# Kernel tuning notes

Measured on AMD Instinct MI355X. Metric: run time of the kernel, lower is better.

The kernel has to match this reference:

```python
import jax, jax.numpy as jnp
import numpy as np

N_NODES = 20000
N_EDGES = 320000
IN_F = 256
HID = 64
OUT_F = 64
EDGE_F = 16
HEADS = 4
NUM_CLASSES = 10
NUM_GRAPHS = 40
ALPHA = 0.2  # LeakyReLU negative slope


def _xavier(key, shape):
    fan_in, fan_out = shape[0], shape[-1]
    std = 1.414 * np.sqrt(2.0 / (fan_in + fan_out))
    return jax.random.normal(key, shape, dtype=jnp.float32) * std


def setup_inputs() -> dict:
    key = jax.random.key(0)
    ks = jax.random.split(key, 12)
    x = jax.random.normal(ks[0], (N_NODES, IN_F), dtype=jnp.float32)
    edge_index = jax.random.randint(ks[1], (2, N_EDGES), 0, N_NODES, dtype=jnp.int32)
    edge_attr = jax.random.uniform(ks[2], (N_EDGES, EDGE_F), dtype=jnp.float32)
    batch = jnp.sort(jax.random.randint(ks[3], (N_NODES,), 0, NUM_GRAPHS, dtype=jnp.int32))
    # layer 0: in=IN_F, heads=HEADS, out=HID, concat
    W0 = _xavier(ks[4], (IN_F, HEADS * HID))
    a0 = _xavier(ks[5], (HEADS, 2 * HID + EDGE_F))
    # layer 1: in=HID*HEADS, heads=HEADS, out=HID, concat
    W1 = _xavier(ks[6], (HID * HEADS, HEADS * HID))
    a1 = _xavier(ks[7], (HEADS, 2 * HID + EDGE_F))
    # layer 2: in=HID*HEADS, heads=1, out=OUT_F, mean over heads
    W2 = _xavier(ks[8], (HID * HEADS, 1 * OUT_F))
    a2 = _xavier(ks[9], (1, 2 * OUT_F + EDGE_F))
    cls_w = _xavier(ks[10], (OUT_F, NUM_CLASSES))
    cls_b = jnp.zeros((NUM_CLASSES,), dtype=jnp.float32)
    return {"x": x, "edge_index": edge_index, "edge_attr": edge_attr, "batch": batch,
            "W0": W0, "a0": a0, "W1": W1, "a1": a1, "W2": W2, "a2": a2,
            "cls_w": cls_w, "cls_b": cls_b}


def gat_layer(h, W, a, edge_index, edge_attr, heads, out_f, concat):
    n = h.shape[0]
    Wh = (h @ W).reshape(n, heads, out_f)              # [N,H,D]
    src, dst = edge_index[0], edge_index[1]
    a_i, a_j, a_e = a[:, :out_f], a[:, out_f:2 * out_f], a[:, 2 * out_f:]
    # per-node head scores, gathered per edge (equivalent to concat + dot with a)
    s_i = jnp.einsum('nhd,hd->nh', Wh, a_i)            # [N,H]
    s_j = jnp.einsum('nhd,hd->nh', Wh, a_j)            # [N,H]
    s_e = edge_attr @ a_e.T                            # [E,H]
    e = s_i[src] + s_j[dst] + s_e                      # [E,H]
    e = jnp.where(e > 0, e, ALPHA * e)                 # LeakyReLU
    # NB: faithful to source — softmax over the HEADS dim (dim=1), not per-node
    att = jax.nn.softmax(e, axis=1)                    # [E,H]
    msg = att[:, :, None] * Wh[dst]                    # [E,H,D]
    h_prime = jax.ops.segment_sum(msg, src, num_segments=n)  # scatter-add to src
    if concat:
        return jax.nn.elu(h_prime.reshape(n, heads * out_f))
    return h_prime.mean(axis=1)


def reference(x, edge_index, edge_attr, batch, W0, a0, W1, a1, W2, a2, cls_w, cls_b):
    h = gat_layer(x, W0, a0, edge_index, edge_attr, HEADS, HID, True)
    h = gat_layer(h, W1, a1, edge_index, edge_attr, HEADS, HID, True)
    h = gat_layer(h, W2, a2, edge_index, edge_attr, 1, OUT_F, False)
    # global mean pool over graphs
    sums = jax.ops.segment_sum(h, batch, num_segments=NUM_GRAPHS)
    cnts = jax.ops.segment_sum(jnp.ones((h.shape[0],), h.dtype), batch, num_segments=NUM_GRAPHS)
    pooled = sums / jnp.maximum(cnts, 1.0)[:, None]
    logits = pooled @ cls_w + cls_b
    return jax.nn.log_softmax(logits, axis=1)
```

## Files before the change

### kernel.cpp

```cpp
#include <hip/hip_runtime.h>
#include <hip/hip_bf16.h>
#include <math.h>

#define N_NODES 20000
#define N_EDGES 320000
#define IN_F 256
#define HID 64
#define HEADS 4
#define OUT_F 64
#define EDGE_F 16
#define NUM_CLASSES 10
#define NUM_GRAPHS 40
#define LRELU_ALPHA 0.2f

typedef short bf16x8 __attribute__((ext_vector_type(8)));
typedef unsigned short u16x8 __attribute__((ext_vector_type(8)));
typedef float f32x4 __attribute__((ext_vector_type(4)));

static __device__ __forceinline__ float bf2f(unsigned short u) {
    union { unsigned int i; float f; } v; v.i = ((unsigned int)u) << 16; return v.f;
}
static __device__ __forceinline__ unsigned short f2bf(float f) {
    union { float f; unsigned int i; } v; v.f = f;
    unsigned int r = v.i + 0x7FFF + ((v.i >> 16) & 1);
    return (unsigned short)(r >> 16);
}
static __device__ __forceinline__ float eluf(float a) {
    return a > 0.f ? a : __expf(a) - 1.0f;
}

__global__ void prep_kernel(const float* __restrict__ W0, const float* __restrict__ W1,
                            const float* __restrict__ W2, unsigned short* __restrict__ W0b,
                            unsigned short* __restrict__ W1b, unsigned short* __restrict__ W2b,
                            int* __restrict__ cnt) {
    int b = blockIdx.x;
    if (b < 144) {
        int i = b * 256 + threadIdx.x;
        const float* src; unsigned short* dst; int off;
        if (i < 16384)      { src = W0; dst = W0b; off = i; }
        else if (i < 32768) { src = W1; dst = W1b; off = i - 16384; }
        else                { src = W2; dst = W2b; off = i - 32768; }
        float4 v = ((const float4*)src)[off];
        ushort4 o;
        o.x = f2bf(v.x); o.y = f2bf(v.y); o.z = f2bf(v.z); o.w = f2bf(v.w);
        ((ushort4*)dst)[off] = o;
    } else {
        int j = (b - 144) * 256 + threadIdx.x;
        if (j < N_NODES / 4) ((int4*)cnt)[j] = make_int4(0, 0, 0, 0);
    }
}

__global__ void count_kernel(const int* __restrict__ src, int* __restrict__ cnt) {
    int e = blockIdx.x * blockDim.x + threadIdx.x;
    if (e < N_EDGES) atomicAdd(&cnt[src[e]], 1);
}

__global__ __launch_bounds__(1024) void scan_kernel(const int* __restrict__ cnt,
                                                    int* __restrict__ row_ptr,
                                                    int* __restrict__ cursor) {
    __shared__ int wsum[16];
    __shared__ int carry_s;
    int t = threadIdx.x;
    int lane = t & 63, wave = t >> 6;
    if (t == 0) { carry_s = 0; row_ptr[0] = 0; }
    __syncthreads();
    for (int base = 0; base < N_NODES; base += 1024) {
        int idx = base + t;
        int x0 = (idx < N_NODES) ? cnt[idx] : 0;
        int x = x0;
#pragma unroll
        for (int off = 1; off < 64; off <<= 1) {
            int y = __shfl_up(x, off, 64);
            if (lane >= off) x += y;
        }
        if (lane == 63) wsum[wave] = x;
        __syncthreads();
        if (wave == 0 && lane < 16) {
            int s = wsum[lane];
#pragma unroll
            for (int off = 1; off < 16; off <<= 1) {
                int y = __shfl_up(s, off, 64);
                if (lane >= off) s += y;
            }
            wsum[lane] = s;
        }
        __syncthreads();
        int waveoff = (wave > 0) ? wsum[wave - 1] : 0;
        int carry = carry_s;
        if (idx < N_NODES) {
            int incl = x + waveoff + carry;
            row_ptr[idx + 1] = incl;
            cursor[idx] = incl - x0;
        }
        __syncthreads();
        if (t == 0) carry_s = carry + wsum[15];
        __syncthreads();
    }
}

__global__ void scatter_kernel(const int* __restrict__ src, const int* __restrict__ dst,
                               const float* __restrict__ ea, const float* __restrict__ a0,
                               const float* __restrict__ a1, int* __restrict__ cursor,
                               int* __restrict__ dstp, float* __restrict__ se0,
                               float* __restrict__ se1) {
    __shared__ float ae[2][4][16];
    int tid = threadIdx.x;
    if (tid < 64) ae[0][tid >> 4][tid & 15] = a0[(tid >> 4) * 144 + 128 + (tid & 15)];
    else if (tid < 128) { int t = tid - 64; ae[1][t >> 4][t & 15] = a1[(t >> 4) * 144 + 128 + (t & 15)]; }
    __syncthreads();
    int e = blockIdx.x * blockDim.x + tid;
    if (e >= N_EDGES) return;
    int s = src[e];
    int pos = atomicAdd(&cursor[s], 1);
    dstp[pos] = dst[e];
    float x[16];
#pragma unroll
    for (int k = 0; k < 16; k += 4) {
        float4 v = *(const float4*)(ea + (size_t)e * 16 + k);
        x[k] = v.x; x[k + 1] = v.y; x[k + 2] = v.z; x[k + 3] = v.w;
    }
    float4 o0 = make_float4(0.f, 0.f, 0.f, 0.f), o1 = o0;
#pragma unroll
    for (int k = 0; k < 16; ++k) {
        o0.x += x[k] * ae[0][0][k]; o0.y += x[k] * ae[0][1][k];
        o0.z += x[k] * ae[0][2][k]; o0.w += x[k] * ae[0][3][k];
        o1.x += x[k] * ae[1][0][k]; o1.y += x[k] * ae[1][1][k];
        o1.z += x[k] * ae[1][2][k]; o1.w += x[k] * ae[1][3][k];
    }
    ((float4*)se0)[pos] = o0;
    ((float4*)se1)[pos] = o1;
}

template <bool AF32, bool SCORES>
__global__ __launch_bounds__(256) void gemm_bf16(const void* __restrict__ Aptr,
                                                 const unsigned short* __restrict__ B,
                                                 unsigned short* __restrict__ C,
                                                 const float* __restrict__ avec,
                                                 float* __restrict__ si, float* __restrict__ sj,
                                                 int M, int N, int K) {
    __shared__ unsigned short As[128][40];
    __shared__ unsigned short Bs[64][40];
    __shared__ unsigned short Cs[128][72];
    __shared__ float sa[128];
    int tid = threadIdx.x;
    if (SCORES && tid < 128) sa[tid] = avec[blockIdx.y * 144 + tid];
    int bm = blockIdx.x * 128, bn = blockIdx.y * 64;
    int w = tid >> 6, l = tid & 63;
    int wr = w * 32;
    int lr = l & 15, lk = (l >> 4) * 8;
    f32x4 acc[2][4] = {};
    int ar = tid >> 1, akc = (tid & 1) * 16;
    int bk = tid >> 3, bn8 = tid & 7, bnc = bn8 * 8;

    for (int k0 = 0; k0 < K; k0 += 32) {
        bf16x8 av0 = {}, av1 = {};
        if (bm + ar < M) {
            if constexpr (AF32) {
                const float* Af = (const float*)Aptr + (size_t)(bm + ar) * K + k0 + akc;
                float4 f0 = ((const float4*)Af)[0];
                float4 f1 = ((const float4*)Af)[1];
                float4 f2 = ((const float4*)Af)[2];
                float4 f3 = ((const float4*)Af)[3];
                av0[0] = (short)f2bf(f0.x); av0[1] = (short)f2bf(f0.y);
                av0[2] = (short)f2bf(f0.z); av0[3] = (short)f2bf(f0.w);
                av0[4] = (short)f2bf(f1.x); av0[5] = (short)f2bf(f1.y);
                av0[6] = (short)f2bf(f1.z); av0[7] = (short)f2bf(f1.w);
                av1[0] = (short)f2bf(f2.x); av1[1] = (short)f2bf(f2.y);
                av1[2] = (short)f2bf(f2.z); av1[3] = (short)f2bf(f2.w);
                av1[4] = (short)f2bf(f3.x); av1[5] = (short)f2bf(f3.y);
                av1[6] = (short)f2bf(f3.z); av1[7] = (short)f2bf(f3.w);
            } else {
                const unsigned short* Ab = (const unsigned short*)Aptr + (size_t)(bm + ar) * K + k0 + akc;
                av0 = *(const bf16x8*)Ab;
                av1 = *(const bf16x8*)(Ab + 8);
            }
        }
        *(bf16x8*)&As[ar][akc] = av0;
        *(bf16x8*)&As[ar][akc + 8] = av1;
        bf16x8 bv = *(const bf16x8*)(B + (size_t)(k0 + bk) * N + bn + bnc);
#pragma unroll
        for (int j = 0; j < 8; ++j) {
            int jj = (j + bn8) & 7;
            Bs[bnc + jj][bk] = (unsigned short)bv[jj];
        }
        __syncthreads();
        bf16x8 a0 = *(const bf16x8*)&As[wr + lr][lk];
        bf16x8 a1 = *(const bf16x8*)&As[wr + 16 + lr][lk];
        bf16x8 b0 = *(const bf16x8*)&Bs[lr][lk];
        bf16x8 b1 = *(const bf16x8*)&Bs[16 + lr][lk];
        bf16x8 b2 = *(const bf16x8*)&Bs[32 + lr][lk];
        bf16x8 b3 = *(const bf16x8*)&Bs[48 + lr][lk];
        acc[0][0] = __builtin_amdgcn_mfma_f32_16x16x32_bf16(a0, b0, acc[0][0], 0, 0, 0);
        acc[0][1] = __builtin_amdgcn_mfma_f32_16x16x32_bf16(a0, b1, acc[0][1], 0, 0, 0);
        acc[0][2] = __builtin_amdgcn_mfma_f32_16x16x32_bf16(a0, b2, acc[0][2], 0, 0, 0);
        acc[0][3] = __builtin_amdgcn_mfma_f32_16x16x32_bf16(a0, b3, acc[0][3], 0, 0, 0);
        acc[1][0] = __builtin_amdgcn_mfma_f32_16x16x32_bf16(a1, b0, acc[1][0], 0, 0, 0);
        acc[1][1] = __builtin_amdgcn_mfma_f32_16x16x32_bf16(a1, b1, acc[1][1], 0, 0, 0);
        acc[1][2] = __builtin_amdgcn_mfma_f32_16x16x32_bf16(a1, b2, acc[1][2], 0, 0, 0);
        acc[1][3] = __builtin_amdgcn_mfma_f32_16x16x32_bf16(a1, b3, acc[1][3], 0, 0, 0);
        __syncthreads();
    }
#pragma unroll
    for (int i = 0; i < 2; ++i)
#pragma unroll
        for (int j = 0; j < 4; ++j)
#pragma unroll
            for (int r = 0; r < 4; ++r)
                Cs[wr + i * 16 + (l >> 4) * 4 + r][j * 16 + (l & 15)] = f2bf(acc[i][j][r]);
    __syncthreads();
    {
        int row = tid >> 3, cc = (tid & 7) * 8;
#pragma unroll
        for (int p = 0; p < 4; ++p, row += 32) {
            if (bm + row < M) {
                bf16x8 o = *(const bf16x8*)&Cs[row][cc];
                *(bf16x8*)(C + (size_t)(bm + row) * N + bn + cc) = o;
            }
        }
    }
    if (SCORES) {
        int r = tid >> 1, half = tid & 1;
        float s0 = 0.f, s1 = 0.f;
#pragma unroll
        for (int k = 0; k < 32; ++k) {
            float f = bf2f(Cs[r][half * 32 + k]);
            s0 += f * sa[half * 32 + k];
            s1 += f * sa[64 + half * 32 + k];
        }
        s0 += __shfl_xor(s0, 1, 64);
        s1 += __shfl_xor(s1, 1, 64);
        if (half == 0 && bm + r < M) {
            si[(size_t)(bm + r) * 4 + blockIdx.y] = s0;
            sj[(size_t)(bm + r) * 4 + blockIdx.y] = s1;
        }
    }
}

__global__ __launch_bounds__(256) void edge_agg_concat(
    const unsigned short* __restrict__ Whb, const float* __restrict__ sev,
    const float* __restrict__ si, const float* __restrict__ sj,
    const int* __restrict__ row_ptr, const int* __restrict__ dstp,
    unsigned short* __restrict__ out) {
    int v = blockIdx.x * 4 + (threadIdx.x >> 6);
    if (v >= N_NODES) return;
    int l = threadIdx.x & 63;
    int slot = l >> 4, p = l & 15;
    int beg = row_ptr[v], end = row_ptr[v + 1];
    float4 si4 = ((const float4*)si)[v];
    float acc0[8] = {}, acc1[8] = {};
    int i = beg + slot;
    int u_n = 0;
    float4 se_n = make_float4(0.f, 0.f, 0.f, 0.f), sj_n = se_n;
    if (i < end) {
        u_n = dstp[i];
        se_n = ((const float4*)sev)[i];
        sj_n = ((const float4*)sj)[u_n];
    }
    for (; i < end; i += 4) {
        int u = u_n;
        float4 se4 = se_n, sj4 = sj_n;
        if (i + 4 < end) {
            u_n = dstp[i + 4];
            se_n = ((const float4*)sev)[i + 4];
            sj_n = ((const float4*)sj)[u_n];
        }
        float t0 = si4.x + sj4.x + se4.x;
        float t1 = si4.y + sj4.y + se4.y;
        float t2 = si4.z + sj4.z + se4.z;
        float t3 = si4.w + sj4.w + se4.w;
        t0 = t0 > 0.f ? t0 : LRELU_ALPHA * t0;
        t1 = t1 > 0.f ? t1 : LRELU_ALPHA * t1;
        t2 = t2 > 0.f ? t2 : LRELU_ALPHA * t2;
        t3 = t3 > 0.f ? t3 : LRELU_ALPHA * t3;
        float m = fmaxf(fmaxf(t0, t1), fmaxf(t2, t3));
        float p0 = __expf(t0 - m), p1 = __expf(t1 - m), p2 = __expf(t2 - m), p3 = __expf(t3 - m);
        float inv = 1.0f / (p0 + p1 + p2 + p3);
        const unsigned short* row = Whb + (size_t)u * 256;
        u16x8 w0 = *(const u16x8*)(row + p * 8);
        u16x8 w1 = *(const u16x8*)(row + 128 + p * 8);
        float atA = ((p & 8) ? p1 : p0) * inv;
        float atB = ((p & 8) ? p3 : p2) * inv;
#pragma unroll
        for (int j = 0; j < 8; ++j) acc0[j] += atA * bf2f(w0[j]);
#pragma unroll
        for (int j = 0; j < 8; ++j) acc1[j] += atB * bf2f(w1[j]);
    }
#pragma unroll
    for (int j = 0; j < 8; ++j) {
        acc0[j] += __shfl_xor(acc0[j], 16, 64);
        acc0[j] += __shfl_xor(acc0[j], 32, 64);
        acc1[j] += __shfl_xor(acc1[j], 16, 64);
        acc1[j] += __shfl_xor(acc1[j], 32, 64);
    }
    if (slot == 0) {
        u16x8 o0, o1;
#pragma unroll
        for (int j = 0; j < 8; ++j) {
            o0[j] = f2bf(eluf(acc0[j]));
            o1[j] = f2bf(eluf(acc1[j]));
        }
        *(u16x8*)(out + (size_t)v * 256 + p * 8) = o0;
        *(u16x8*)(out + (size_t)v * 256 + 128 + p * 8) = o1;
    }
}

__global__ __launch_bounds__(256) void edge_agg_single(
    const unsigned short* __restrict__ Whb, const int* __restrict__ row_ptr,
    const int* __restrict__ dstp, float* __restrict__ out) {
    int v = blockIdx.x * 4 + (threadIdx.x >> 6);
    if (v >= N_NODES) return;
    int l = threadIdx.x & 63;
    int slot = l >> 3, p = l & 7;
    int beg = row_ptr[v], end = row_ptr[v + 1];
    float acc[8] = {};
    int i = beg + slot;
    int u_n = 0;
    if (i < end) u_n = dstp[i];
    for (; i < end; i += 8) {
        int u = u_n;
        if (i + 8 < end) u_n = dstp[i + 8];
        u16x8 w = *(const u16x8*)(Whb + (size_t)u * 64 + p * 8);
#pragma unroll
        for (int j = 0; j < 8; ++j) acc[j] += bf2f(w[j]);
    }
#pragma unroll
    for (int j = 0; j < 8; ++j) {
        acc[j] += __shfl_xor(acc[j], 8, 64);
        acc[j] += __shfl_xor(acc[j], 16, 64);
        acc[j] += __shfl_xor(acc[j], 32, 64);
    }
    if (l < 8) {
        float4 o0 = make_float4(acc[0], acc[1], acc[2], acc[3]);
        float4 o1 = make_float4(acc[4], acc[5], acc[6], acc[7]);
        *(float4*)(out + (size_t)v * 64 + p * 8) = o0;
        *(float4*)(out + (size_t)v * 64 + p * 8 + 4) = o1;
    }
}

__global__ __launch_bounds__(1024) void pool_kernel(const float* __restrict__ h3,
                                                    const int* __restrict__ batch,
                                                    float* __restrict__ pooled) {
    int g = blockIdx.x;
    int lane = threadIdx.x & 63;
    int wave = threadIdx.x >> 6;
    int lo = 0, hi = N_NODES;
    while (lo < hi) { int mid = (lo + hi) >> 1; if (batch[mid] < g) lo = mid + 1; else hi = mid; }
    int start = lo;
    lo = start; hi = N_NODES;
    while (lo < hi) { int mid = (lo + hi) >> 1; if (batch[mid] < g + 1) lo = mid + 1; else hi = mid; }
    int endi = lo;
    float s = 0.f;
    for (int v = start + wave; v < endi; v += 16) s += h3[(size_t)v * 64 + lane];
    __shared__ float red[16][64];
    red[wave][lane] = s;
    __syncthreads();
    if (wave == 0) {
        float t = red[0][lane];
#pragma unroll
        for (int w = 1; w < 16; ++w) t += red[w][lane];
        float c = (float)((endi - start) > 1 ? (endi - start) : 1);
        pooled[g * 64 + lane] = t / c;
    }
}

__global__ void classify_kernel(const float* __restrict__ pooled, const float* __restrict__ cw,
                                const float* __restrict__ cb, float* __restrict__ out) {
    int g = threadIdx.x;
    if (g >= NUM_GRAPHS) return;
    float lg[NUM_CLASSES];
#pragma unroll
    for (int c = 0; c < NUM_CLASSES; ++c) lg[c] = cb[c];
    for (int d = 0; d < OUT_F; ++d) {
        float p = pooled[g * 64 + d];
#pragma unroll
        for (int c = 0; c < NUM_CLASSES; ++c) lg[c] += p * cw[d * NUM_CLASSES + c];
    }
    float m = lg[0];
#pragma unroll
    for (int c = 1; c < NUM_CLASSES; ++c) m = fmaxf(m, lg[c]);
    float s = 0.f;
#pragma unroll
    for (int c = 0; c < NUM_CLASSES; ++c) s += expf(lg[c] - m);
    float lse = m + logf(s);
#pragma unroll
    for (int c = 0; c < NUM_CLASSES; ++c) out[g * NUM_CLASSES + c] = lg[c] - lse;
}

extern "C" void kernel_launch(void* const* d_in, const int* in_sizes, int n_in,
                              void* d_out, int out_size, void* d_ws, size_t ws_size,
                              hipStream_t stream) {
    const float* x   = (const float*)d_in[0];
    const int*   ei  = (const int*)d_in[1];
    const float* ea  = (const float*)d_in[2];
    const int* batch = (const int*)d_in[3];
    const float* W0  = (const float*)d_in[4];
    const float* a0  = (const float*)d_in[5];
    const float* W1  = (const float*)d_in[6];
    const float* a1  = (const float*)d_in[7];
    const float* W2  = (const float*)d_in[8];
    const float* cw  = (const float*)d_in[10];
    const float* cb  = (const float*)d_in[11];
    float* out = (float*)d_out;

    const int* srcg = ei;
    const int* dstg = ei + N_EDGES;

    char* ws = (char*)d_ws;
    size_t off = 0;
    auto alloc = [&](size_t bytes) -> char* {
        char* p = ws + off;
        off += (bytes + 255) & ~(size_t)255;
        return p;
    };
    unsigned short* W0b  = (unsigned short*)alloc(256 * 256 * 2);
    unsigned short* W1b  = (unsigned short*)alloc(256 * 256 * 2);
    unsigned short* W2b  = (unsigned short*)alloc(256 * 64 * 2);
    unsigned short* Whb  = (unsigned short*)alloc((size_t)N_NODES * 256 * 2);
    unsigned short* hAb  = (unsigned short*)alloc((size_t)N_NODES * 256 * 2);
    unsigned short* hBb  = (unsigned short*)alloc((size_t)N_NODES * 256 * 2);
    unsigned short* Wh2b = (unsigned short*)alloc((size_t)N_NODES * 64 * 2);
    float* si   = (float*)alloc((size_t)N_NODES * HEADS * 4);
    float* sj   = (float*)alloc((size_t)N_NODES * HEADS * 4);
    float* se0  = (float*)alloc((size_t)N_EDGES * HEADS * 4);
    float* se1  = (float*)alloc((size_t)N_EDGES * HEADS * 4);
    int* row_ptr = (int*)alloc((N_NODES + 1) * 4);
    int* cursor  = (int*)alloc(N_NODES * 4);
    int* cnt  = (int*)alloc(N_NODES * 4);
    int* dstp = (int*)alloc(N_EDGES * 4);
    float* h3 = (float*)alloc((size_t)N_NODES * 64 * 4);
    float* pooled = (float*)alloc(NUM_GRAPHS * 64 * 4);

    prep_kernel<<<144 + (N_NODES / 4 + 255) / 256, 256, 0, stream>>>(W0, W1, W2, W0b, W1b, W2b, cnt);

    count_kernel<<<(N_EDGES + 255) / 256, 256, 0, stream>>>(srcg, cnt);
    scan_kernel<<<1, 1024, 0, stream>>>(cnt, row_ptr, cursor);
    scatter_kernel<<<(N_EDGES + 255) / 256, 256, 0, stream>>>(srcg, dstg, ea, a0, a1, cursor,
                                                              dstp, se0, se1);

    dim3 ggrid((N_NODES + 127) / 128, 4);
    dim3 ggrid2((N_NODES + 127) / 128, 1);
    int agb = (N_NODES + 3) / 4;

    gemm_bf16<true, true><<<ggrid, 256, 0, stream>>>(x, W0b, Whb, a0, si, sj, N_NODES, 256, 256);
    edge_agg_concat<<<agb, 256, 0, stream>>>(Whb, se0, si, sj, row_ptr, dstp, hAb);

    gemm_bf16<false, true><<<ggrid, 256, 0, stream>>>(hAb, W1b, Whb, a1, si, sj, N_NODES, 256, 256);
    edge_agg_concat<<<agb, 256, 0, stream>>>(Whb, se1, si, sj, row_ptr, dstp, hBb);

    gemm_bf16<false, false><<<ggrid2, 256, 0, stream>>>(hBb, W2b, Wh2b, nullptr, nullptr, nullptr,
                                                        N_NODES, 64, 256);
    edge_agg_single<<<agb, 256, 0, stream>>>(Wh2b, row_ptr, dstp, h3);

    pool_kernel<<<NUM_GRAPHS, 1024, 0, stream>>>(h3, batch, pooled);
    classify_kernel<<<1, 64, 0, stream>>>(pooled, cw, cb, out);
}
```

Before: 207.8 us.

## Prefetch gathered rows in edge aggregation, interleave edge scores, vectorize counting

The concat aggregation kernel now gives each lane 8 contiguous features out of 256 and runs two edge slots per wave instead of four. The next edge's feature row is prefetched one iteration ahead, and its index and score two ahead, so the dependent gather latency overlaps with compute. The per-layer edge scores are stored interleaved in one buffer, and count_kernel reads four source indices per thread. The single-head aggregation gets the same row prefetch. The aim is to hide gather latency at the cost of more registers and fewer edges in flight per wave; interleaving the scores also makes each layer's score loads strided.

Result: slower. 227.9 us (+9.7%).

```diff
diff --git a/kernel.cpp b/kernel.cpp
--- a/kernel.cpp
+++ b/kernel.cpp
@@ -50,9 +50,15 @@
     }
 }
 
-__global__ void count_kernel(const int* __restrict__ src, int* __restrict__ cnt) {
-    int e = blockIdx.x * blockDim.x + threadIdx.x;
-    if (e < N_EDGES) atomicAdd(&cnt[src[e]], 1);
+__global__ void count_kernel(const int4* __restrict__ src4, int* __restrict__ cnt) {
+    int i = blockIdx.x * blockDim.x + threadIdx.x;
+    if (i < N_EDGES / 4) {
+        int4 s = src4[i];
+        atomicAdd(&cnt[s.x], 1);
+        atomicAdd(&cnt[s.y], 1);
+        atomicAdd(&cnt[s.z], 1);
+        atomicAdd(&cnt[s.w], 1);
+    }
 }
 
 __global__ __launch_bounds__(1024) void scan_kernel(const int* __restrict__ cnt,
@@ -101,8 +107,7 @@
 __global__ void scatter_kernel(const int* __restrict__ src, const int* __restrict__ dst,
                                const float* __restrict__ ea, const float* __restrict__ a0,
                                const float* __restrict__ a1, int* __restrict__ cursor,
-                               int* __restrict__ dstp, float* __restrict__ se0,
-                               float* __restrict__ se1) {
+                               int* __restrict__ dstp, float* __restrict__ se01) {
     __shared__ float ae[2][4][16];
     int tid = threadIdx.x;
     if (tid < 64) ae[0][tid >> 4][tid & 15] = a0[(tid >> 4) * 144 + 128 + (tid & 15)];
@@ -127,8 +132,8 @@
         o1.x += x[k] * ae[1][0][k]; o1.y += x[k] * ae[1][1][k];
         o1.z += x[k] * ae[1][2][k]; o1.w += x[k] * ae[1][3][k];
     }
-    ((float4*)se0)[pos] = o0;
-    ((float4*)se1)[pos] = o1;
+    ((float4*)se01)[(size_t)pos * 2]     = o0;
+    ((float4*)se01)[(size_t)pos * 2 + 1] = o1;
 }
 
 template <bool AF32, bool SCORES>
@@ -237,37 +242,49 @@
 }
 
 __global__ __launch_bounds__(256) void edge_agg_concat(
-    const unsigned short* __restrict__ Whb, const float* __restrict__ sev,
+    const unsigned short* __restrict__ Whb, const float4* __restrict__ sev,
     const float* __restrict__ si, const float* __restrict__ sj,
     const int* __restrict__ row_ptr, const int* __restrict__ dstp,
     unsigned short* __restrict__ out) {
     int v = blockIdx.x * 4 + (threadIdx.x >> 6);
     if (v >= N_NODES) return;
     int l = threadIdx.x & 63;
-    int slot = l >> 4, p = l & 15;
+    int slot = l >> 5;
+    int p = l & 31;
     int beg = row_ptr[v], end = row_ptr[v + 1];
     float4 si4 = ((const float4*)si)[v];
-    float acc0[8] = {}, acc1[8] = {};
+    float acc[8] = {};
     int i = beg + slot;
+    int u_c = 0;
+    float4 se_c = make_float4(0.f, 0.f, 0.f, 0.f), sj_c = se_c;
+    u16x8 w_c = {};
+    if (i < end) {
+        u_c = dstp[i];
+        se_c = sev[(size_t)i * 2];
+        sj_c = ((const float4*)sj)[u_c];
+        w_c = *(const u16x8*)(Whb + (size_t)u_c * 256 + p * 8);
+    }
     int u_n = 0;
     float4 se_n = make_float4(0.f, 0.f, 0.f, 0.f), sj_n = se_n;
-    if (i < end) {
-        u_n = dstp[i];
-        se_n = ((const float4*)sev)[i];
+    if (i + 2 < end) {
+        u_n = dstp[i + 2];
+        se_n = sev[(size_t)(i + 2) * 2];
         sj_n = ((const float4*)sj)[u_n];
     }
-    for (; i < end; i += 4) {
-        int u = u_n;
-        float4 se4 = se_n, sj4 = sj_n;
+    for (; i < end; i += 2) {
+        u16x8 w_n = {};
+        if (i + 2 < end) w_n = *(const u16x8*)(Whb + (size_t)u_n * 256 + p * 8);
+        int u_nn = 0;
+        float4 se_nn = make_float4(0.f, 0.f, 0.f, 0.f), sj_nn = se_nn;
         if (i + 4 < end) {
-            u_n = dstp[i + 4];
-            se_n = ((const float4*)sev)[i + 4];
-            sj_n = ((const float4*)sj)[u_n];
-        }
-        float t0 = si4.x + sj4.x + se4.x;
-        float t1 = si4.y + sj4.y + se4.y;
-        float t2 = si4.z + sj4.z + se4.z;
-        float t3 = si4.w + sj4.w + se4.w;
+            u_nn = dstp[i + 4];
+            se_nn = sev[(size_t)(i + 4) * 2];
+            sj_nn = ((const float4*)sj)[u_nn];
+        }
+        float t0 = si4.x + sj_c.x + se_c.x;
+        float t1 = si4.y + sj_c.y + se_c.y;
+        float t2 = si4.z + sj_c.z + se_c.z;
+        float t3 = si4.w + sj_c.w + se_c.w;
         t0 = t0 > 0.f ? t0 : LRELU_ALPHA * t0;
         t1 = t1 > 0.f ? t1 : LRELU_ALPHA * t1;
         t2 = t2 > 0.f ? t2 : LRELU_ALPHA * t2;
@@ -275,32 +292,19 @@
         float m = fmaxf(fmaxf(t0, t1), fmaxf(t2, t3));
         float p0 = __expf(t0 - m), p1 = __expf(t1 - m), p2 = __expf(t2 - m), p3 = __expf(t3 - m);
         float inv = 1.0f / (p0 + p1 + p2 + p3);
-        const unsigned short* row = Whb + (size_t)u * 256;
-        u16x8 w0 = *(const u16x8*)(row + p * 8);
-        u16x8 w1 = *(const u16x8*)(row + 128 + p * 8);
-        float atA = ((p & 8) ? p1 : p0) * inv;
-        float atB = ((p & 8) ? p3 : p2) * inv;
-#pragma unroll
-        for (int j = 0; j < 8; ++j) acc0[j] += atA * bf2f(w0[j]);
-#pragma unroll
-        for (int j = 0; j < 8; ++j) acc1[j] += atB * bf2f(w1[j]);
-    }
-#pragma unroll
-    for (int j = 0; j < 8; ++j) {
-        acc0[j] += __shfl_xor(acc0[j], 16, 64);
-        acc0[j] += __shfl_xor(acc0[j], 32, 64);
-        acc1[j] += __shfl_xor(acc1[j], 16, 64);
-        acc1[j] += __shfl_xor(acc1[j], 32, 64);
-    }
+        float at = ((p & 16) ? ((p & 8) ? p3 : p2) : ((p & 8) ? p1 : p0)) * inv;
+#pragma unroll
+        for (int j = 0; j < 8; ++j) acc[j] += at * bf2f(w_c[j]);
+        u_c = u_n; se_c = se_n; sj_c = sj_n; w_c = w_n;
+        u_n = u_nn; se_n = se_nn; sj_n = sj_nn;
+    }
+#pragma unroll
+    for (int j = 0; j < 8; ++j) acc[j] += __shfl_xor(acc[j], 32, 64);
     if (slot == 0) {
-        u16x8 o0, o1;
-#pragma unroll
-        for (int j = 0; j < 8; ++j) {
-            o0[j] = f2bf(eluf(acc0[j]));
-            o1[j] = f2bf(eluf(acc1[j]));
-        }
-        *(u16x8*)(out + (size_t)v * 256 + p * 8) = o0;
-        *(u16x8*)(out + (size_t)v * 256 + 128 + p * 8) = o1;
+        u16x8 o;
+#pragma unroll
+        for (int j = 0; j < 8; ++j) o[j] = f2bf(eluf(acc[j]));
+        *(u16x8*)(out + (size_t)v * 256 + p * 8) = o;
     }
 }
 
@@ -314,14 +318,22 @@
     int beg = row_ptr[v], end = row_ptr[v + 1];
     float acc[8] = {};
     int i = beg + slot;
+    int u_c = 0;
+    u16x8 w_c = {};
+    if (i < end) {
+        u_c = dstp[i];
+        w_c = *(const u16x8*)(Whb + (size_t)u_c * 64 + p * 8);
+    }
     int u_n = 0;
-    if (i < end) u_n = dstp[i];
+    if (i + 8 < end) u_n = dstp[i + 8];
     for (; i < end; i += 8) {
-        int u = u_n;
-        if (i + 8 < end) u_n = dstp[i + 8];
-        u16x8 w = *(const u16x8*)(Whb + (size_t)u * 64 + p * 8);
-#pragma unroll
-        for (int j = 0; j < 8; ++j) acc[j] += bf2f(w[j]);
+        u16x8 w_n = {};
+        if (i + 8 < end) w_n = *(const u16x8*)(Whb + (size_t)u_n * 64 + p * 8);
+        int u_nn = 0;
+        if (i + 16 < end) u_nn = dstp[i + 16];
+#pragma unroll
+        for (int j = 0; j < 8; ++j) acc[j] += bf2f(w_c[j]);
+        w_c = w_n; u_n = u_nn;
     }
 #pragma unroll
     for (int j = 0; j < 8; ++j) {
@@ -421,8 +433,7 @@
     unsigned short* Wh2b = (unsigned short*)alloc((size_t)N_NODES * 64 * 2);
     float* si   = (float*)alloc((size_t)N_NODES * HEADS * 4);
     float* sj   = (float*)alloc((size_t)N_NODES * HEADS * 4);
-    float* se0  = (float*)alloc((size_t)N_EDGES * HEADS * 4);
-    float* se1  = (float*)alloc((size_t)N_EDGES * HEADS * 4);
+    float* se01 = (float*)alloc((size_t)N_EDGES * 8 * 4);
     int* row_ptr = (int*)alloc((N_NODES + 1) * 4);
     int* cursor  = (int*)alloc(N_NODES * 4);
     int* cnt  = (int*)alloc(N_NODES * 4);
@@ -432,20 +443,20 @@
 
     prep_kernel<<<144 + (N_NODES / 4 + 255) / 256, 256, 0, stream>>>(W0, W1, W2, W0b, W1b, W2b, cnt);
 
-    count_kernel<<<(N_EDGES + 255) / 256, 256, 0, stream>>>(srcg, cnt);
+    count_kernel<<<(N_EDGES / 4 + 255) / 256, 256, 0, stream>>>((const int4*)srcg, cnt);
     scan_kernel<<<1, 1024, 0, stream>>>(cnt, row_ptr, cursor);
     scatter_kernel<<<(N_EDGES + 255) / 256, 256, 0, stream>>>(srcg, dstg, ea, a0, a1, cursor,
-                                                              dstp, se0, se1);
+                                                              dstp, se01);
 
     dim3 ggrid((N_NODES + 127) / 128, 4);
     dim3 ggrid2((N_NODES + 127) / 128, 1);
     int agb = (N_NODES + 3) / 4;
 
     gemm_bf16<true, true><<<ggrid, 256, 0, stream>>>(x, W0b, Whb, a0, si, sj, N_NODES, 256, 256);
-    edge_agg_concat<<<agb, 256, 0, stream>>>(Whb, se0, si, sj, row_ptr, dstp, hAb);
+    edge_agg_concat<<<agb, 256, 0, stream>>>(Whb, (const float4*)se01, si, sj, row_ptr, dstp, hAb);
 
     gemm_bf16<false, true><<<ggrid, 256, 0, stream>>>(hAb, W1b, Whb, a1, si, sj, N_NODES, 256, 256);
-    edge_agg_concat<<<agb, 256, 0, stream>>>(Whb, se1, si, sj, row_ptr, dstp, hBb);
+    edge_agg_concat<<<agb, 256, 0, stream>>>(Whb, (const float4*)se01 + 1, si, sj, row_ptr, dstp, hBb);
 
     gemm_bf16<false, false><<<ggrid2, 256, 0, stream>>>(hBb, W2b, Wh2b, nullptr, nullptr, nullptr,
                                                         N_NODES, 64, 256);
```

## Split attention softmax into separate edge-parallel kernel and vectorize edge counting

Applied to the files above, without the earlier changes.

Moves the per-edge LeakyReLU/softmax attention computation out of the aggregation loop into a new edge-parallel att_kernel that writes normalized attention per sorted edge. The aggregation kernel then loads only dst index and a precomputed float4, which removes the dependent sj gather and the exp math from its latency-bound loop. The scatter now also records sorted src, and the two layers' edge scores are interleaved into one buffer. The count kernel reads four src indices per thread as an int4. This adds two extra launches and extra global traffic for the attention buffer.

Measured after the change: 205.8 us. About the same (-0.9%).

```diff
diff --git a/kernel.cpp b/kernel.cpp
--- a/kernel.cpp
+++ b/kernel.cpp
@@ -50,9 +50,15 @@
     }
 }
 
-__global__ void count_kernel(const int* __restrict__ src, int* __restrict__ cnt) {
-    int e = blockIdx.x * blockDim.x + threadIdx.x;
-    if (e < N_EDGES) atomicAdd(&cnt[src[e]], 1);
+__global__ void count_kernel(const int4* __restrict__ src4, int* __restrict__ cnt) {
+    int i = blockIdx.x * blockDim.x + threadIdx.x;
+    if (i < N_EDGES / 4) {
+        int4 s = src4[i];
+        atomicAdd(&cnt[s.x], 1);
+        atomicAdd(&cnt[s.y], 1);
+        atomicAdd(&cnt[s.z], 1);
+        atomicAdd(&cnt[s.w], 1);
+    }
 }
 
 __global__ __launch_bounds__(1024) void scan_kernel(const int* __restrict__ cnt,
@@ -101,8 +107,8 @@
 __global__ void scatter_kernel(const int* __restrict__ src, const int* __restrict__ dst,
                                const float* __restrict__ ea, const float* __restrict__ a0,
                                const float* __restrict__ a1, int* __restrict__ cursor,
-                               int* __restrict__ dstp, float* __restrict__ se0,
-                               float* __restrict__ se1) {
+                               int* __restrict__ srcp, int* __restrict__ dstp,
+                               float* __restrict__ se01) {
     __shared__ float ae[2][4][16];
     int tid = threadIdx.x;
     if (tid < 64) ae[0][tid >> 4][tid & 15] = a0[(tid >> 4) * 144 + 128 + (tid & 15)];
@@ -112,6 +118,7 @@
     if (e >= N_EDGES) return;
     int s = src[e];
     int pos = atomicAdd(&cursor[s], 1);
+    srcp[pos] = s;
     dstp[pos] = dst[e];
     float x[16];
 #pragma unroll
@@ -127,8 +134,8 @@
         o1.x += x[k] * ae[1][0][k]; o1.y += x[k] * ae[1][1][k];
         o1.z += x[k] * ae[1][2][k]; o1.w += x[k] * ae[1][3][k];
     }
-    ((float4*)se0)[pos] = o0;
-    ((float4*)se1)[pos] = o1;
+    ((float4*)se01)[(size_t)pos * 2]     = o0;
+    ((float4*)se01)[(size_t)pos * 2 + 1] = o1;
 }
 
 template <bool AF32, bool SCORES>
@@ -236,9 +243,31 @@
     }
 }
 
+__global__ void att_kernel(const int* __restrict__ srcp, const int* __restrict__ dstp,
+                           const float4* __restrict__ sev, const float* __restrict__ si,
+                           const float* __restrict__ sj, float4* __restrict__ attp) {
+    int i = blockIdx.x * blockDim.x + threadIdx.x;
+    if (i >= N_EDGES) return;
+    int s = srcp[i], u = dstp[i];
+    float4 siv = ((const float4*)si)[s];
+    float4 sjv = ((const float4*)sj)[u];
+    float4 se4 = sev[(size_t)i * 2];
+    float t0 = siv.x + sjv.x + se4.x;
+    float t1 = siv.y + sjv.y + se4.y;
+    float t2 = siv.z + sjv.z + se4.z;
+    float t3 = siv.w + sjv.w + se4.w;
+    t0 = t0 > 0.f ? t0 : LRELU_ALPHA * t0;
+    t1 = t1 > 0.f ? t1 : LRELU_ALPHA * t1;
+    t2 = t2 > 0.f ? t2 : LRELU_ALPHA * t2;
+    t3 = t3 > 0.f ? t3 : LRELU_ALPHA * t3;
+    float m = fmaxf(fmaxf(t0, t1), fmaxf(t2, t3));
+    float p0 = __expf(t0 - m), p1 = __expf(t1 - m), p2 = __expf(t2 - m), p3 = __expf(t3 - m);
+    float inv = 1.0f / (p0 + p1 + p2 + p3);
+    attp[i] = make_float4(p0 * inv, p1 * inv, p2 * inv, p3 * inv);
+}
+
 __global__ __launch_bounds__(256) void edge_agg_concat(
-    const unsigned short* __restrict__ Whb, const float* __restrict__ sev,
-    const float* __restrict__ si, const float* __restrict__ sj,
+    const unsigned short* __restrict__ Whb, const float4* __restrict__ attp,
     const int* __restrict__ row_ptr, const int* __restrict__ dstp,
     unsigned short* __restrict__ out) {
     int v = blockIdx.x * 4 + (threadIdx.x >> 6);
@@ -246,40 +275,20 @@
     int l = threadIdx.x & 63;
     int slot = l >> 4, p = l & 15;
     int beg = row_ptr[v], end = row_ptr[v + 1];
-    float4 si4 = ((const float4*)si)[v];
     float acc0[8] = {}, acc1[8] = {};
     int i = beg + slot;
     int u_n = 0;
-    float4 se_n = make_float4(0.f, 0.f, 0.f, 0.f), sj_n = se_n;
-    if (i < end) {
-        u_n = dstp[i];
-        se_n = ((const float4*)sev)[i];
-        sj_n = ((const float4*)sj)[u_n];
-    }
+    float4 at_n = make_float4(0.f, 0.f, 0.f, 0.f);
+    if (i < end) { u_n = dstp[i]; at_n = attp[i]; }
     for (; i < end; i += 4) {
         int u = u_n;
-        float4 se4 = se_n, sj4 = sj_n;
-        if (i + 4 < end) {
-            u_n = dstp[i + 4];
-            se_n = ((const float4*)sev)[i + 4];
-            sj_n = ((const float4*)sj)[u_n];
-        }
-        float t0 = si4.x + sj4.x + se4.x;
-        float t1 = si4.y + sj4.y + se4.y;
-        float t2 = si4.z + sj4.z + se4.z;
-        float t3 = si4.w + sj4.w + se4.w;
-        t0 = t0 > 0.f ? t0 : LRELU_ALPHA * t0;
-        t1 = t1 > 0.f ? t1 : LRELU_ALPHA * t1;
-        t2 = t2 > 0.f ? t2 : LRELU_ALPHA * t2;
-        t3 = t3 > 0.f ? t3 : LRELU_ALPHA * t3;
-        float m = fmaxf(fmaxf(t0, t1), fmaxf(t2, t3));
-        float p0 = __expf(t0 - m), p1 = __expf(t1 - m), p2 = __expf(t2 - m), p3 = __expf(t3 - m);
-        float inv = 1.0f / (p0 + p1 + p2 + p3);
+        float4 at4 = at_n;
+        if (i + 4 < end) { u_n = dstp[i + 4]; at_n = attp[i + 4]; }
         const unsigned short* row = Whb + (size_t)u * 256;
         u16x8 w0 = *(const u16x8*)(row + p * 8);
         u16x8 w1 = *(const u16x8*)(row + 128 + p * 8);
-        float atA = ((p & 8) ? p1 : p0) * inv;
-        float atB = ((p & 8) ? p3 : p2) * inv;
+        float atA = (p & 8) ? at4.y : at4.x;
+        float atB = (p & 8) ? at4.w : at4.z;
 #pragma unroll
         for (int j = 0; j < 8; ++j) acc0[j] += atA * bf2f(w0[j]);
 #pragma unroll
@@ -421,31 +430,35 @@
     unsigned short* Wh2b = (unsigned short*)alloc((size_t)N_NODES * 64 * 2);
     float* si   = (float*)alloc((size_t)N_NODES * HEADS * 4);
     float* sj   = (float*)alloc((size_t)N_NODES * HEADS * 4);
-    float* se0  = (float*)alloc((size_t)N_EDGES * HEADS * 4);
-    float* se1  = (float*)alloc((size_t)N_EDGES * HEADS * 4);
+    float* se01 = (float*)alloc((size_t)N_EDGES * 8 * 4);
+    float* attp = (float*)alloc((size_t)N_EDGES * HEADS * 4);
     int* row_ptr = (int*)alloc((N_NODES + 1) * 4);
     int* cursor  = (int*)alloc(N_NODES * 4);
     int* cnt  = (int*)alloc(N_NODES * 4);
+    int* srcp = (int*)alloc(N_EDGES * 4);
     int* dstp = (int*)alloc(N_EDGES * 4);
     float* h3 = (float*)alloc((size_t)N_NODES * 64 * 4);
     float* pooled = (float*)alloc(NUM_GRAPHS * 64 * 4);
 
     prep_kernel<<<144 + (N_NODES / 4 + 255) / 256, 256, 0, stream>>>(W0, W1, W2, W0b, W1b, W2b, cnt);
 
-    count_kernel<<<(N_EDGES + 255) / 256, 256, 0, stream>>>(srcg, cnt);
+    count_kernel<<<(N_EDGES / 4 + 255) / 256, 256, 0, stream>>>((const int4*)srcg, cnt);
     scan_kernel<<<1, 1024, 0, stream>>>(cnt, row_ptr, cursor);
     scatter_kernel<<<(N_EDGES + 255) / 256, 256, 0, stream>>>(srcg, dstg, ea, a0, a1, cursor,
-                                                              dstp, se0, se1);
+                                                              srcp, dstp, se01);
 
     dim3 ggrid((N_NODES + 127) / 128, 4);
     dim3 ggrid2((N_NODES + 127) / 128, 1);
+    int atb = (N_EDGES + 255) / 256;
     int agb = (N_NODES + 3) / 4;
 
     gemm_bf16<true, true><<<ggrid, 256, 0, stream>>>(x, W0b, Whb, a0, si, sj, N_NODES, 256, 256);
-    edge_agg_concat<<<agb, 256, 0, stream>>>(Whb, se0, si, sj, row_ptr, dstp, hAb);
+    att_kernel<<<atb, 256, 0, stream>>>(srcp, dstp, (const float4*)se01, si, sj, (float4*)attp);
+    edge_agg_concat<<<agb, 256, 0, stream>>>(Whb, (const float4*)attp, row_ptr, dstp, hAb);
 
     gemm_bf16<false, true><<<ggrid, 256, 0, stream>>>(hAb, W1b, Whb, a1, si, sj, N_NODES, 256, 256);
-    edge_agg_concat<<<agb, 256, 0, stream>>>(Whb, se1, si, sj, row_ptr, dstp, hBb);
+    att_kernel<<<atb, 256, 0, stream>>>(srcp, dstp, (const float4*)se01 + 1, si, sj, (float4*)attp);
+    edge_agg_concat<<<agb, 256, 0, stream>>>(Whb, (const float4*)attp, row_ptr, dstp, hBb);
 
     gemm_bf16<false, false><<<ggrid2, 256, 0, stream>>>(hBb, W2b, Wh2b, nullptr, nullptr, nullptr,
                                                         N_NODES, 64, 256);
```
